# Kernel optimization log

Hardware: AMD Instinct MI355X
Metric: run time of the kernel (lower is better)

## Reference

```python
import jax, jax.numpy as jnp
import numpy as np

B, SEQ, NVAR, DM, K = 2, 512, 64, 128, 2
SCALE = DM ** -0.5  # ScaledDotProductAttention scale, lsa=False so constant


def _period_branch(x4, Wel, bel, Wq, bq, Wk, bk, Wv, bv, Wo, bo, period):
    # x4: [B, DM(time), NVAR, DM(dim)] -- output of start_embed
    pad = (-DM) % period
    pn = (DM + pad) // period  # period_num
    xp = jnp.pad(x4, ((0, 0), (0, pad), (0, 0), (0, 0)))
    # torch .unfold(dim=1, size=period, step=period) -> [B, pn, NVAR, DM, period]
    xw = xp.reshape(B, pn, period, NVAR, DM).transpose(0, 1, 3, 4, 2)
    # emb_linear over the d_model (dim) axis
    xw = jnp.einsum('bqndl,ed->bqnel', xw, Wel) + bel[None, None, None, :, None]
    # -> [B, NVAR, dim, pn, period] then flatten to conv1d layout [bn, dim, L]
    X = xw.transpose(0, 2, 3, 1, 4).reshape(B * NVAR, DM, pn * period)
    # 1x1 Conv1d QKV projections over the channel (dim) axis
    q = jnp.einsum('bdl,ed->bel', X, Wq) + bq[None, :, None]
    k = jnp.einsum('bdl,ed->bel', X, Wk) + bk[None, :, None]
    v = jnp.einsum('bdl,ed->bel', X, Wv) + bv[None, :, None]
    q_s = q.reshape(B * NVAR, DM, pn, period).transpose(0, 1, 3, 2)  # [bn,dim,pl,pn]
    k_s = k.reshape(B * NVAR, DM, pn, period)                         # [bn,dim,pn,pl]
    v_s = v.reshape(B * NVAR, DM, pn, period).transpose(0, 1, 3, 2)  # [bn,dim,pl,pn]
    attn = jax.nn.softmax(jnp.einsum('bdip,bdpj->bdij', q_s, k_s) * SCALE, axis=-1)
    o = jnp.einsum('bdij,bdjp->bdip', attn, v_s)  # [bn, dim, period, pn]
    o = o.reshape(B * NVAR, DM, period * pn)[:, :, :DM]  # truncate to n_heads=DM
    return o @ Wo.T + bo  # to_out Linear(n_heads, n_heads), dropout eval-mode


def reference(x, W_emb, b_emb, W_start, b_start, Wel, bel, Wq, bq, Wk, bk, Wv, bv, Wo, bo, f1, f2):
    # inverted embedding: Linear(seq_len->d_model) over time, then permute -> [B, DM, NVAR]
    xe = (jnp.einsum('bsn,sd->bnd', x, W_emb) + b_emb).transpose(0, 2, 1)
    # FFT_for_Period amplitudes; top-k frequency indices f1,f2 are static (host-side in torch)
    amp = jnp.abs(jnp.fft.rfft(xe, axis=1)).mean(-1)  # [B, DM//2+1]
    pw = jax.nn.softmax(jnp.stack([amp[:, f1], amp[:, f2]], -1), axis=-1)  # [B, K]
    # start_embed: Linear(1 -> d_model) -> [B, DM, NVAR, DM]
    x4 = xe[..., None] * W_start + b_start
    outs = [_period_branch(x4, Wel, bel, Wq, bq, Wk, bk, Wv, bv, Wo, bo, DM // f)
            for f in (f1, f2)]
    res = jnp.stack(outs, -1)                      # [B*NVAR, DM, DM, K]
    pw_b = jnp.repeat(pw, NVAR, axis=0)            # [B*NVAR, K] (b-major order matches reshape)
    out = (res * pw_b[:, None, None, :]).sum(-1)
    return out.reshape(B, NVAR, DM, DM)


def setup_inputs() -> dict:
    key = jax.random.key(0)
    ks = jax.random.split(key, 16)
    s = 0.02
    d = {
        'x': jax.random.normal(ks[0], (B, SEQ, NVAR), jnp.float32),
        'W_emb': jax.random.normal(ks[1], (SEQ, DM), jnp.float32) * s,
        'b_emb': jax.random.normal(ks[2], (DM,), jnp.float32) * s,
        'W_start': jax.random.normal(ks[3], (DM,), jnp.float32) * s,
        'b_start': jax.random.normal(ks[4], (DM,), jnp.float32) * s,
        'Wel': jax.random.normal(ks[5], (DM, DM), jnp.float32) * s,
        'bel': jax.random.normal(ks[6], (DM,), jnp.float32) * s,
        'Wq': jax.random.normal(ks[7], (DM, DM), jnp.float32) * s,
        'bq': jax.random.normal(ks[8], (DM,), jnp.float32) * s,
        'Wk': jax.random.normal(ks[9], (DM, DM), jnp.float32) * s,
        'bk': jax.random.normal(ks[10], (DM,), jnp.float32) * s,
        'Wv': jax.random.normal(ks[11], (DM, DM), jnp.float32) * s,
        'bv': jax.random.normal(ks[12], (DM,), jnp.float32) * s,
        'Wo': jax.random.normal(ks[13], (DM, DM), jnp.float32) * s,
        'bo': jax.random.normal(ks[14], (DM,), jnp.float32) * s,
    }
    # host-side FFT period detection, mirroring torch's .detach().cpu().numpy() topk
    xe = np.einsum('bsn,sd->bnd', np.asarray(d['x']), np.asarray(d['W_emb'])) + np.asarray(d['b_emb'])
    xe = xe.transpose(0, 2, 1)  # [B, DM, NVAR]
    fl = np.abs(np.fft.rfft(xe, axis=1)).mean(0).mean(-1)
    fl[0] = 0.0
    top = np.argsort(-fl, kind='stable')[:K]
    d['f1'] = int(top[0])
    d['f2'] = int(top[1])
    return d
```

## Files before the change

### kernel.cpp

```cpp
#include <hip/hip_runtime.h>

#define DMD 128
#define NV 64
#define BB 2
#define SQ 512
#define NBN 128
#define ASCALE 0.08838834764831845f
#define L2E 1.4426950408889634f
#define CSC (ASCALE * L2E)

#define WS_XE  0
#define WS_PW  (WS_XE + NBN*DMD)
#define WS_VEC (WS_PW + 4)
#define WS_OB  (WS_VEC + 9*DMD)

__global__ __launch_bounds__(512) void k_xe(const float* __restrict__ x,
                                            const float* __restrict__ W_emb,
                                            const float* __restrict__ b_emb,
                                            float* __restrict__ ws) {
    int bn = blockIdx.x;
    int b = bn >> 6, n = bn & 63;
    int tid = threadIdx.x;
    int t = tid & 127, sc = tid >> 7;
    __shared__ float xsh[SQ];
    __shared__ float part[3][DMD];
    xsh[tid] = x[(b * SQ + tid) * NV + n];
    __syncthreads();
    float acc = 0.f;
    const float* W = W_emb + (sc * 128) * DMD + t;
#pragma unroll 8
    for (int s = 0; s < 128; ++s) acc = fmaf(xsh[sc * 128 + s], W[s * DMD], acc);
    if (sc) part[sc - 1][t] = acc;
    __syncthreads();
    if (sc == 0)
        ws[WS_XE + bn * DMD + t] = acc + part[0][t] + part[1][t] + part[2][t] + b_emb[t];
}

__global__ __launch_bounds__(128) void k_prep(const int* __restrict__ f1p,
                                              const int* __restrict__ f2p,
                                              const float* __restrict__ Wel, const float* __restrict__ bel,
                                              const float* __restrict__ W_start, const float* __restrict__ b_start,
                                              const float* __restrict__ Wq, const float* __restrict__ bq,
                                              const float* __restrict__ Wk, const float* __restrict__ bk,
                                              const float* __restrict__ Wv, const float* __restrict__ bv,
                                              float* __restrict__ ws) {
    int tid = threadIdx.x;
    __shared__ float ct[DMD], st[DMD];
    __shared__ float a2[2];
    __shared__ float A[DMD], C[DMD], BL[DMD];
    if (blockIdx.x < 2) {
        int b = blockIdx.x;
        float ang = (float)tid * 0.04908738521234052f;
        ct[tid] = cosf(ang);
        st[tid] = sinf(ang);
        __syncthreads();
        int k = tid >> 6;
        int n = tid & 63;
        int f = k ? f2p[0] : f1p[0];
        const float* xr = ws + WS_XE + (b * NV + n) * DMD;
        float re = 0.f, im = 0.f;
        for (int t = 0; t < DMD; ++t) {
            int ph = (f * t) & (DMD - 1);
            float v = xr[t];
            re = fmaf(v, ct[ph], re);
            im = fmaf(v, st[ph], im);
        }
        float amp = sqrtf(re * re + im * im);
        for (int off = 32; off > 0; off >>= 1) amp += __shfl_down(amp, off);
        if (n == 0) a2[k] = amp * (1.0f / NV);
        __syncthreads();
        if (tid == 0) {
            float m = fmaxf(a2[0], a2[1]);
            float e0 = expf(a2[0] - m), e1 = expf(a2[1] - m);
            float inv = 1.0f / (e0 + e1);
            ws[WS_PW + b * 2 + 0] = e0 * inv;
            ws[WS_PW + b * 2 + 1] = e1 * inv;
        }
    } else {
        int e = tid;
        float a = 0.f, c = 0.f;
        for (int d = 0; d < DMD; ++d) {
            float w = Wel[e * DMD + d];
            a = fmaf(w, W_start[d], a);
            c = fmaf(w, b_start[d], c);
        }
        A[e] = a;
        C[e] = c + bel[e];
        BL[e] = bel[e];
        __syncthreads();
        float aq = 0, cq = 0, pq = 0, ak = 0, ck = 0, pk = 0, av = 0, cv = 0, pv = 0;
        for (int d = 0; d < DMD; ++d) {
            float Ad = A[d], Cd = C[d], Bd = BL[d];
            float wq = Wq[e * DMD + d], wk = Wk[e * DMD + d], wv = Wv[e * DMD + d];
            aq = fmaf(wq, Ad, aq); cq = fmaf(wq, Cd, cq); pq = fmaf(wq, Bd, pq);
            ak = fmaf(wk, Ad, ak); ck = fmaf(wk, Cd, ck); pk = fmaf(wk, Bd, pk);
            av = fmaf(wv, Ad, av); cv = fmaf(wv, Cd, cv); pv = fmaf(wv, Bd, pv);
        }
        float* V = ws + WS_VEC;
        V[0 * DMD + e] = aq; V[1 * DMD + e] = cq + bq[e]; V[2 * DMD + e] = pq + bq[e];
        V[3 * DMD + e] = ak; V[4 * DMD + e] = ck + bk[e]; V[5 * DMD + e] = pk + bk[e];
        V[6 * DMD + e] = av; V[7 * DMD + e] = cv + bv[e]; V[8 * DMD + e] = pv + bv[e];
    }
}


__device__ __forceinline__ void attn_rank1(int br, float pwv, const float (*Vsh)[4],
                                           const float* xs, float (*obuf)[132], int tid) {
    float xi = xs[tid];
    float t[4], l[4], ax[4];
#pragma unroll
    for (int k = 0; k < 4; ++k) {
        float Aq = Vsh[0][k], Cq = Vsh[1][k], Ak = Vsh[3][k];
        t[k] = CSC * fmaf(xi, Aq, Cq) * Ak;
        l[k] = 0.f; ax[k] = 0.f;
    }
#pragma unroll 4
    for (int j = 0; j < DMD; ++j) {
        float xj = xs[j];
#pragma unroll
        for (int k = 0; k < 4; ++k) {
            float ev = exp2f(t[k] * xj);
            l[k] += ev;
            ax[k] = fmaf(ev, xj, ax[k]);
        }
    }
#pragma unroll
    for (int k = 0; k < 4; ++k) {
        float Av = Vsh[6][k], Cv = Vsh[7][k];
        float o = fmaf(Av, ax[k] / l[k], Cv);
        float val = pwv * o;
        if (br == 0) obuf[k][tid] = val; else obuf[k][tid] += val;
    }
}

template<int PP, int NP>
__device__ __forceinline__ void attn_pow2(int br, float pwv, const float (*Vsh)[4],
                                          const float* xs, float (*obuf)[132], int tid) {
    const int UH = PP / 4;
    int lane4 = tid & 3, i0 = tid >> 2, jb = lane4 * UH;

    float xq[NP][UH], U2[UH];
#pragma unroll
    for (int u = 0; u < UH; ++u) {
        int j = jb + u;
        float s = 0.f;
#pragma unroll
        for (int q = 0; q < NP; ++q) { float xv = xs[q * PP + j]; xq[q][u] = xv; s += xv; }
        U2[u] = s;
    }
    const int NREP = (PP == 64) ? 2 : 1;
#pragma unroll
    for (int rep = 0; rep < NREP; ++rep) {
        int i = i0 + rep * 32;
        float G2[UH];
#pragma unroll
        for (int u = 0; u < UH; ++u) G2[u] = 0.f;
#pragma unroll
        for (int q = 0; q < NP; ++q) {
            float xi = xs[q * PP + i];
#pragma unroll
            for (int u = 0; u < UH; ++u) G2[u] = fmaf(xi, xq[q][u], G2[u]);
        }
        for (int ec = 0; ec < 4; ++ec) {
            float Aq = Vsh[0][ec], Cq = Vsh[1][ec];
            float Ak = Vsh[3][ec];
            float Av = Vsh[6][ec], Cv = Vsh[7][ec];
            float t = CSC * Ak;
            float d1 = t * Aq, d2 = t * Cq;
            float l0 = 0.f, l1 = 0.f;
            float accq[NP];
#pragma unroll
            for (int q = 0; q < NP; ++q) accq[q] = 0.f;
#pragma unroll
            for (int u = 0; u < UH; ++u) {
                float ev = exp2f(fmaf(d1, G2[u], d2 * U2[u]));
                if (u & 1) l1 += ev; else l0 += ev;
#pragma unroll
                for (int q = 0; q < NP; ++q) accq[q] = fmaf(ev, xq[q][u], accq[q]);
            }
            float l = l0 + l1;
            l += __shfl_xor(l, 1); l += __shfl_xor(l, 2);
#pragma unroll
            for (int q = 0; q < NP; ++q) {
                accq[q] += __shfl_xor(accq[q], 1);
                accq[q] += __shfl_xor(accq[q], 2);
            }
            if (lane4 == 0) {
                float li = 1.f / l;
#pragma unroll
                for (int q = 0; q < NP; ++q) {
                    float o = fmaf(Av, accq[q] * li, Cv);
                    float val = pwv * o;
                    int mo = i * NP + q;
                    if (br == 0) obuf[ec][mo] = val; else obuf[ec][mo] += val;
                }
            }
        }
    }
}

template<int UB>
__device__ __forceinline__ void attn_small(
    int P, int pn, int r, int Prows, int br, float pwv,
    const float (*Vsh)[4], const float* xs, const float* U, const float* xt,
    float* W, float (*obuf)[132], int tid)
{
    int GP = P + 1;
    int tot = Prows * P;
    unsigned mP = (4096u + (unsigned)P - 1u) / (unsigned)P;
    unsigned mpn = (4096u + (unsigned)pn - 1u) / (unsigned)pn;

    bool v0 = (tid < tot);
    int i0 = (int)(((unsigned)tid * mP) >> 12);
    int j0 = tid - i0 * P;
    bool A0 = (i0 < r), c0 = (j0 < r);
    float xtj0 = xt[j0], Uj0 = U[j0];
    float xti0 = A0 ? xt[i0] : 0.f;
    float g0 = 0.f;
    for (int p = 0; p < pn - 1; ++p) g0 = fmaf(xs[p * P + i0], xs[p * P + j0], g0);
    float Gx0 = (A0 && c0) ? fmaf(xti0, xtj0, g0) : g0;
    float Ux0 = (A0 && c0) ? Uj0 + xtj0 : Uj0;
    float Xw0 = (!A0 && c0) ? xtj0 : 0.f;
    float mw0 = c0 ? 1.f : 0.f;
    int wa0 = i0 * GP + j0;

    int idx1 = tid + 128;
    bool v1 = (idx1 < tot);
    int idx1c = v1 ? idx1 : 0;
    int i1 = (int)(((unsigned)idx1c * mP) >> 12);
    int j1 = idx1c - i1 * P;
    bool A1 = (i1 < r), c1 = (j1 < r);
    float xtj1 = xt[j1], Uj1 = U[j1];
    float xti1 = A1 ? xt[i1] : 0.f;
    float g1 = 0.f;
    for (int p = 0; p < pn - 1; ++p) g1 = fmaf(xs[p * P + i1], xs[p * P + j1], g1);
    float Gx1 = (A1 && c1) ? fmaf(xti1, xtj1, g1) : g1;
    float Ux1 = (A1 && c1) ? Uj1 + xtj1 : Uj1;
    float Xw1 = (!A1 && c1) ? xtj1 : 0.f;
    float mw1 = c1 ? 1.f : 0.f;
    int wa1 = i1 * GP + j1;

    int i2 = (int)(((unsigned)tid * mpn) >> 12);
    int p2 = tid - i2 * pn;
    bool lastp = (p2 == pn - 1);
    int row2 = i2 * GP;
    float xsr[UB];
#pragma unroll
    for (int j = 0; j < UB; ++j) {
        int idx = p2 * P + j;
        xsr[j] = (j < P && idx < DMD) ? xs[idx] : 0.f;
    }

    for (int ec = 0; ec < 4; ++ec) {
        float Aq = Vsh[0][ec], Cq = Vsh[1][ec], Pq = Vsh[2][ec];
        float Ak = Vsh[3][ec], Ck = Vsh[4][ec], Pk = Vsh[5][ec];
        float Av = Vsh[6][ec], Cv = Vsh[7][ec], Pv = Vsh[8][ec];
        float t = CSC * Ak;
        float d1 = t * Aq, d2 = t * Cq, d3 = t * Pq;
        float ckpk = CSC * (Ck - Pk);

        if (v0) {
            float aS = A0 ? fmaf(Aq, xti0, Cq) : Pq;
            float S = (ckpk * aS) * mw0;
            S = fmaf(d3, Xw0, S);
            S = fmaf(d2, Ux0, S);
            S = fmaf(d1, Gx0, S);
            W[wa0] = exp2f(S);
        }
        if (v1) {
            float aS = A1 ? fmaf(Aq, xti1, Cq) : Pq;
            float S = (ckpk * aS) * mw1;
            S = fmaf(d3, Xw1, S);
            S = fmaf(d2, Ux1, S);
            S = fmaf(d1, Gx1, S);
            W[wa1] = exp2f(S);
        }
        __syncthreads();
        float l = 0.f, wr = 0.f, ax = 0.f;
#pragma unroll
        for (int j = 0; j < UB; ++j) {
            float w = W[row2 + ((j < P) ? j : 0)];
            w = (j < P) ? w : 0.f;
            l += w;
            wr += (j < r) ? w : 0.f;
            ax = fmaf(w, xsr[j], ax);
        }
        float li = 1.f / l;
        float o;
        if (lastp) { float sl = wr * li; o = fmaf(Av, ax * li, fmaf(Cv, sl, Pv * (1.f - sl))); }
        else       o = fmaf(Av, ax * li, Cv);
        float val = pwv * o;
        if (br == 0) obuf[ec][tid] = val; else obuf[ec][tid] += val;
        __syncthreads();
    }
}

template<int UH, int NP>
__device__ __forceinline__ void attn_midA(
    int P, int pn, int r, int Prows, int br, float pwv,
    const float (*Vsh)[4], const float* xs, const float* U,
    const float* xt, float (*obuf)[132], int tid)
{
    int lane4 = tid & 3;
    int i0 = tid >> 2;
    int jb = lane4 * UH;

    float Ur[UH], xtr[UH], xq0[UH], xq1[UH];
#pragma unroll
    for (int u = 0; u < UH; ++u) {
        int j = jb + u, jc = (j < P) ? j : 0;
        Ur[u] = U[jc];
        xtr[u] = xt[jc];
        xq0[u] = (j < DMD) ? xs[j] : 0.f;
        int i1x = P + j;
        xq1[u] = (i1x < DMD) ? xs[i1x] : 0.f;
    }
    int nrep = (Prows > 32) ? 2 : 1;
    for (int rep = 0; rep < nrep; ++rep) {
        int i = i0 + rep * 32;
        bool rowact = (i < Prows);
        int ic = rowact ? i : 0;
        float xtic = xt[ic];
        bool rowvalid = (ic < r);
        float g[UH];
#pragma unroll
        for (int u = 0; u < UH; ++u) g[u] = 0.f;
        for (int p = 0; p < pn - 1; ++p) {
            float xi = xs[p * P + ic];
#pragma unroll
            for (int u = 0; u < UH; ++u) {
                int j = jb + u, jc = (j < P) ? j : 0;
                g[u] = fmaf(xi, xs[p * P + jc], g[u]);
            }
        }
        for (int ec = 0; ec < 4; ++ec) {
            float Aq = Vsh[0][ec], Cq = Vsh[1][ec], Pq = Vsh[2][ec];
            float Ak = Vsh[3][ec], Ck = Vsh[4][ec], Pk = Vsh[5][ec];
            float Av = Vsh[6][ec], Cv = Vsh[7][ec], Pv = Vsh[8][ec];
            float c1 = CSC * Aq * Ak, c3 = CSC * Cq * Ak;
            float asi = CSC * (rowvalid ? fmaf(xtic, Aq, Cq) : Pq);

            float l0 = 0.f, l1 = 0.f, w0 = 0.f, w1 = 0.f;
            float accq[NP];
#pragma unroll
            for (int q = 0; q < NP; ++q) accq[q] = 0.f;
#pragma unroll
            for (int u = 0; u < UH; ++u) {
                int j = jb + u;
                float bK = (j < r) ? fmaf(xtr[u], Ak, Ck) : Pk;
                float S = fmaf(asi, bK, fmaf(c3, Ur[u], c1 * g[u]));
                float ev = exp2f(S);
                ev = (j < P) ? ev : 0.f;
                if (u & 1) l1 += ev; else l0 += ev;
                float evr = (j < r) ? ev : 0.f;
                if (u & 1) w1 += evr; else w0 += evr;
                accq[0] = fmaf(ev, xq0[u], accq[0]);
                if (NP >= 2) accq[1] = fmaf(ev, xq1[u], accq[1]);
#pragma unroll
                for (int q = 2; q < NP; ++q) {
                    int idx = q * P + j;
                    float xv = (idx < DMD) ? xs[idx] : 0.f;
                    accq[q] = fmaf(ev, xv, accq[q]);
                }
            }
            float l = l0 + l1, wr = w0 + w1;
            l += __shfl_xor(l, 1);  l += __shfl_xor(l, 2);
            wr += __shfl_xor(wr, 1); wr += __shfl_xor(wr, 2);
#pragma unroll
            for (int q = 0; q < NP; ++q) {
                if (q < pn) {
                    accq[q] += __shfl_xor(accq[q], 1);
                    accq[q] += __shfl_xor(accq[q], 2);
                }
            }
            if (lane4 == 0 && rowact) {
                float li = 1.f / l;
#pragma unroll
                for (int q = 0; q < NP; ++q) {
                    if (q < pn) {
                        int mo = i * pn + q;
                        if (mo < DMD) {
                            float o;
                            if (q == pn - 1) {
                                float sl = wr * li;
                                o = fmaf(Av, accq[q] * li, fmaf(Cv, sl, Pv * (1.f - sl)));
                            } else {
                                o = fmaf(Av, accq[q] * li, Cv);
                            }
                            float val = pwv * o;
                            if (br == 0) obuf[ec][mo] = val;
                            else         obuf[ec][mo] += val;
                        }
                    }
                }
            }
        }
    }
}

__global__ __launch_bounds__(128) void k_attn(const int* __restrict__ f1p,
                                              const int* __restrict__ f2p,
                                              float* __restrict__ ws) {
    int bn = blockIdx.y, b = bn >> 6;
    int e0 = blockIdx.x * 4;
    int tid = threadIdx.x;

    __shared__ float xs[DMD], U[64], xt[64];
    __shared__ float Vsh[9][4];
    __shared__ float W[288];
    __shared__ float obuf[4][132];

    xs[tid] = ws[WS_XE + bn * DMD + tid];
    if (tid < 36) Vsh[tid >> 2][tid & 3] = ws[WS_VEC + (tid >> 2) * DMD + e0 + (tid & 3)];
    int fv0 = f1p[0], fv1 = f2p[0];
    float pw0 = ws[WS_PW + b * 2 + 0];
    float pw1 = ws[WS_PW + b * 2 + 1];
    __syncthreads();

    for (int br = 0; br < 2; ++br) {
        int f = br ? fv1 : fv0;
        float pwv = br ? pw1 : pw0;
        int P = DMD / f;
        int pn = (DMD + P - 1) / P;
        int r = DMD - (pn - 1) * P;
        int Prows = (DMD + pn - 1) / pn;

        if (br == 1) __syncthreads();

        if (P == DMD) {
            attn_rank1(br, pwv, Vsh, xs, obuf, tid);
        } else {
            if (tid < P) {
                float s = 0.f;
                for (int p = 0; p < pn - 1; ++p) s += xs[p * P + tid];
                U[tid] = s;
                xt[tid] = (tid < r) ? xs[(pn - 1) * P + tid] : 0.f;
            }
            __syncthreads();
            if (P <= 4)       attn_small<4>(P, pn, r, Prows, br, pwv, Vsh, xs, U, xt, W, obuf, tid);
            else if (P <= 8)  attn_small<8>(P, pn, r, Prows, br, pwv, Vsh, xs, U, xt, W, obuf, tid);
            else if (P <= 16) attn_small<16>(P, pn, r, Prows, br, pwv, Vsh, xs, U, xt, W, obuf, tid);
            else if (P == 64) attn_pow2<64, 2>(br, pwv, Vsh, xs, obuf, tid);
            else if (P == 32) attn_pow2<32, 4>(br, pwv, Vsh, xs, obuf, tid);
            else if (P > 32)  attn_midA<16, 4>(P, pn, r, Prows, br, pwv, Vsh, xs, U, xt, obuf, tid);
            else              attn_midA<8, 8>(P, pn, r, Prows, br, pwv, Vsh, xs, U, xt, obuf, tid);
        }
    }
    __syncthreads();
    for (int ec = 0; ec < 4; ++ec)
        ws[WS_OB + (bn * DMD + e0 + ec) * DMD + tid] = obuf[ec][tid];
}

__global__ __launch_bounds__(256) void k_out(const float* __restrict__ Wo,
                                             const float* __restrict__ bo,
                                             const float* __restrict__ ws,
                                             float* __restrict__ out) {
    int blk = blockIdx.x;
    int bn0 = (blk >> 2) * 2;
    int e0  = (blk & 3) * 32;
    int tid = threadIdx.x;
    __shared__ __align__(16) float WTc[32 * 132];
    __shared__ __align__(16) float oT[2][32][36];
    int hg = tid & 31, eg = tid >> 5, h0 = hg * 4;

    float acc[2][4][4];
#pragma unroll
    for (int a = 0; a < 2; ++a)
#pragma unroll
        for (int c = 0; c < 4; ++c)
#pragma unroll
            for (int d = 0; d < 4; ++d) acc[a][c][d] = 0.f;

    for (int mc = 0; mc < 4; ++mc) {
        int m0 = mc * 32;
        __syncthreads();
        for (int idx = tid; idx < 4096; idx += 256) {
            int h = idx >> 5, mm = idx & 31;
            WTc[mm * 132 + h] = Wo[h * DMD + m0 + mm];
        }
        for (int idx = tid; idx < 2048; idx += 256) {
            int bnl = idx >> 10, rem = idx & 1023, e = rem >> 5, mm = rem & 31;
            oT[bnl][mm][e] = ws[WS_OB + ((bn0 + bnl) * DMD + e0 + e) * DMD + m0 + mm];
        }
        __syncthreads();
#pragma unroll 4
        for (int mm = 0; mm < 32; ++mm) {
            const float4 wv = *reinterpret_cast<const float4*>(&WTc[mm * 132 + h0]);
            const float4 q0 = *reinterpret_cast<const float4*>(&oT[0][mm][eg * 4]);
            const float4 q1 = *reinterpret_cast<const float4*>(&oT[1][mm][eg * 4]);
            float ae[2][4] = {{q0.x, q0.y, q0.z, q0.w}, {q1.x, q1.y, q1.z, q1.w}};
#pragma unroll
            for (int bnl = 0; bnl < 2; ++bnl) {
#pragma unroll
                for (int el = 0; el < 4; ++el) {
                    float a = ae[bnl][el];
                    acc[bnl][el][0] = fmaf(a, wv.x, acc[bnl][el][0]);
                    acc[bnl][el][1] = fmaf(a, wv.y, acc[bnl][el][1]);
                    acc[bnl][el][2] = fmaf(a, wv.z, acc[bnl][el][2]);
                    acc[bnl][el][3] = fmaf(a, wv.w, acc[bnl][el][3]);
                }
            }
        }
    }
    const float4 bov = *reinterpret_cast<const float4*>(&bo[h0]);
#pragma unroll
    for (int bnl = 0; bnl < 2; ++bnl) {
#pragma unroll
        for (int el = 0; el < 4; ++el) {
            float4 res = { acc[bnl][el][0] + bov.x, acc[bnl][el][1] + bov.y,
                           acc[bnl][el][2] + bov.z, acc[bnl][el][3] + bov.w };
            int e = e0 + eg * 4 + el;
            *reinterpret_cast<float4*>(&out[((bn0 + bnl) * DMD + e) * DMD + h0]) = res;
        }
    }
}

extern "C" void kernel_launch(void* const* d_in, const int* in_sizes, int n_in,
                              void* d_out, int out_size, void* d_ws, size_t ws_size,
                              hipStream_t stream) {
    const float* x       = (const float*)d_in[0];
    const float* W_emb   = (const float*)d_in[1];
    const float* b_emb   = (const float*)d_in[2];
    const float* W_start = (const float*)d_in[3];
    const float* b_start = (const float*)d_in[4];
    const float* Wel     = (const float*)d_in[5];
    const float* bel     = (const float*)d_in[6];
    const float* Wq      = (const float*)d_in[7];
    const float* bq      = (const float*)d_in[8];
    const float* Wk      = (const float*)d_in[9];
    const float* bk      = (const float*)d_in[10];
    const float* Wv      = (const float*)d_in[11];
    const float* bv      = (const float*)d_in[12];
    const float* Wo      = (const float*)d_in[13];
    const float* bo      = (const float*)d_in[14];
    const int*   f1p     = (const int*)d_in[15];
    const int*   f2p     = (const int*)d_in[16];
    float* ws  = (float*)d_ws;
    float* out = (float*)d_out;

    k_xe<<<NBN, 512, 0, stream>>>(x, W_emb, b_emb, ws);
    k_prep<<<3, 128, 0, stream>>>(f1p, f2p, Wel, bel, W_start, b_start,
                                  Wq, bq, Wk, bk, Wv, bv, ws);
    k_attn<<<dim3(32, NBN), 128, 0, stream>>>(f1p, f2p, ws);
    k_out<<<256, 256, 0, stream>>>(Wo, bo, ws, out);
}
```

Baseline: 81.95 us.

## Split attention branches across grid z and write partials directly to global

The two period branches now run in separate blocks along a third grid dimension instead of sequentially in one block. Each branch writes its weighted output straight to global memory, one to the workspace and one to the output buffer, and k_out sums the two partials when loading. attn_small computes all four channels' scores before a single barrier, and attn_pow2 handles several channels per pass. This doubles parallelism and removes shared-memory accumulation and barriers, at the cost of an extra global read in k_out and the output buffer serving as scratch.

```diff
diff --git a/kernel.cpp b/kernel.cpp
--- a/kernel.cpp
+++ b/kernel.cpp
@@ -59,6 +59,7 @@
         int f = k ? f2p[0] : f1p[0];
         const float* xr = ws + WS_XE + (b * NV + n) * DMD;
         float re = 0.f, im = 0.f;
+#pragma unroll 8
         for (int t = 0; t < DMD; ++t) {
             int ph = (f * t) & (DMD - 1);
             float v = xr[t];
@@ -104,8 +105,9 @@
 }
 
 
-__device__ __forceinline__ void attn_rank1(int br, float pwv, const float (*Vsh)[4],
-                                           const float* xs, float (*obuf)[132], int tid) {
+__device__ __forceinline__ void attn_rank1(float pwv, const float (*Vsh)[4],
+                                           const float* xs, float* __restrict__ ob,
+                                           int rowbase, int tid) {
     float xi = xs[tid];
     float t[4], l[4], ax[4];
 #pragma unroll
@@ -128,14 +130,14 @@
     for (int k = 0; k < 4; ++k) {
         float Av = Vsh[6][k], Cv = Vsh[7][k];
         float o = fmaf(Av, ax[k] / l[k], Cv);
-        float val = pwv * o;
-        if (br == 0) obuf[k][tid] = val; else obuf[k][tid] += val;
-    }
-}
-
-template<int PP, int NP>
-__device__ __forceinline__ void attn_pow2(int br, float pwv, const float (*Vsh)[4],
-                                          const float* xs, float (*obuf)[132], int tid) {
+        ob[rowbase + k * DMD + tid] = pwv * o;
+    }
+}
+
+template<int PP, int NP, int EB>
+__device__ __forceinline__ void attn_pow2(float pwv, const float (*Vsh)[4],
+                                          const float* xs, float* __restrict__ ob,
+                                          int rowbase, int tid) {
     const int UH = PP / 4;
     int lane4 = tid & 3, i0 = tid >> 2, jb = lane4 * UH;
 
@@ -161,38 +163,51 @@
 #pragma unroll
             for (int u = 0; u < UH; ++u) G2[u] = fmaf(xi, xq[q][u], G2[u]);
         }
-        for (int ec = 0; ec < 4; ++ec) {
-            float Aq = Vsh[0][ec], Cq = Vsh[1][ec];
-            float Ak = Vsh[3][ec];
-            float Av = Vsh[6][ec], Cv = Vsh[7][ec];
-            float t = CSC * Ak;
-            float d1 = t * Aq, d2 = t * Cq;
-            float l0 = 0.f, l1 = 0.f;
-            float accq[NP];
-#pragma unroll
-            for (int q = 0; q < NP; ++q) accq[q] = 0.f;
+#pragma unroll
+        for (int eg = 0; eg < 4; eg += EB) {
+            float d1[EB], d2[EB], l[EB];
+            float accq[NP][EB];
+#pragma unroll
+            for (int k = 0; k < EB; ++k) {
+                float t = CSC * Vsh[3][eg + k];
+                d1[k] = t * Vsh[0][eg + k];
+                d2[k] = t * Vsh[1][eg + k];
+                l[k] = 0.f;
+#pragma unroll
+                for (int q = 0; q < NP; ++q) accq[q][k] = 0.f;
+            }
 #pragma unroll
             for (int u = 0; u < UH; ++u) {
-                float ev = exp2f(fmaf(d1, G2[u], d2 * U2[u]));
-                if (u & 1) l1 += ev; else l0 += ev;
-#pragma unroll
-                for (int q = 0; q < NP; ++q) accq[q] = fmaf(ev, xq[q][u], accq[q]);
-            }
-            float l = l0 + l1;
-            l += __shfl_xor(l, 1); l += __shfl_xor(l, 2);
-#pragma unroll
-            for (int q = 0; q < NP; ++q) {
-                accq[q] += __shfl_xor(accq[q], 1);
-                accq[q] += __shfl_xor(accq[q], 2);
-            }
+                float gg = G2[u], uu = U2[u];
+                float ev[EB];
+#pragma unroll
+                for (int k = 0; k < EB; ++k) ev[k] = exp2f(fmaf(d1[k], gg, d2[k] * uu));
+#pragma unroll
+                for (int k = 0; k < EB; ++k) {
+                    l[k] += ev[k];
+#pragma unroll
+                    for (int q = 0; q < NP; ++q) accq[q][k] = fmaf(ev[k], xq[q][u], accq[q][k]);
+                }
+            }
+#pragma unroll
+            for (int k = 0; k < EB; ++k) { l[k] += __shfl_xor(l[k], 1); l[k] += __shfl_xor(l[k], 2); }
+#pragma unroll
+            for (int q = 0; q < NP; ++q)
+#pragma unroll
+                for (int k = 0; k < EB; ++k) {
+                    accq[q][k] += __shfl_xor(accq[q][k], 1);
+                    accq[q][k] += __shfl_xor(accq[q][k], 2);
+                }
             if (lane4 == 0) {
-                float li = 1.f / l;
-#pragma unroll
-                for (int q = 0; q < NP; ++q) {
-                    float o = fmaf(Av, accq[q] * li, Cv);
-                    float val = pwv * o;
-                    int mo = i * NP + q;
-                    if (br == 0) obuf[ec][mo] = val; else obuf[ec][mo] += val;
+#pragma unroll
+                for (int k = 0; k < EB; ++k) {
+                    float li = 1.f / l[k];
+                    float Av = Vsh[6][eg + k], Cv = Vsh[7][eg + k];
+#pragma unroll
+                    for (int q = 0; q < NP; ++q) {
+                        float o = fmaf(Av, accq[q][k] * li, Cv);
+                        ob[rowbase + (eg + k) * DMD + i * NP + q] = pwv * o;
+                    }
                 }
             }
         }
@@ -201,9 +216,9 @@
 
 template<int UB>
 __device__ __forceinline__ void attn_small(
-    int P, int pn, int r, int Prows, int br, float pwv,
+    int P, int pn, int r, int Prows, float pwv,
     const float (*Vsh)[4], const float* xs, const float* U, const float* xt,
-    float* W, float (*obuf)[132], int tid)
+    float* W, float* __restrict__ ob, int rowbase, int tid)
 {
     int GP = P + 1;
     int tot = Prows * P;
@@ -251,35 +266,35 @@
         xsr[j] = (j < P && idx < DMD) ? xs[idx] : 0.f;
     }
 
+    float s[4][2];
+#pragma unroll
     for (int ec = 0; ec < 4; ++ec) {
         float Aq = Vsh[0][ec], Cq = Vsh[1][ec], Pq = Vsh[2][ec];
         float Ak = Vsh[3][ec], Ck = Vsh[4][ec], Pk = Vsh[5][ec];
-        float Av = Vsh[6][ec], Cv = Vsh[7][ec], Pv = Vsh[8][ec];
         float t = CSC * Ak;
         float d1 = t * Aq, d2 = t * Cq, d3 = t * Pq;
         float ckpk = CSC * (Ck - Pk);
-
-        if (v0) {
-            float aS = A0 ? fmaf(Aq, xti0, Cq) : Pq;
-            float S = (ckpk * aS) * mw0;
-            S = fmaf(d3, Xw0, S);
-            S = fmaf(d2, Ux0, S);
-            S = fmaf(d1, Gx0, S);
-            W[wa0] = exp2f(S);
-        }
-        if (v1) {
-            float aS = A1 ? fmaf(Aq, xti1, Cq) : Pq;
-            float S = (ckpk * aS) * mw1;
-            S = fmaf(d3, Xw1, S);
-            S = fmaf(d2, Ux1, S);
-            S = fmaf(d1, Gx1, S);
-            W[wa1] = exp2f(S);
-        }
-        __syncthreads();
+        float aS0 = A0 ? fmaf(Aq, xti0, Cq) : Pq;
+        s[ec][0] = fmaf(d1, Gx0, fmaf(d2, Ux0, fmaf(d3, Xw0, (ckpk * aS0) * mw0)));
+        float aS1 = A1 ? fmaf(Aq, xti1, Cq) : Pq;
+        s[ec][1] = fmaf(d1, Gx1, fmaf(d2, Ux1, fmaf(d3, Xw1, (ckpk * aS1) * mw1)));
+    }
+#pragma unroll
+    for (int ec = 0; ec < 4; ++ec) { s[ec][0] = exp2f(s[ec][0]); s[ec][1] = exp2f(s[ec][1]); }
+#pragma unroll
+    for (int ec = 0; ec < 4; ++ec) {
+        if (v0) W[ec * 288 + wa0] = s[ec][0];
+        if (v1) W[ec * 288 + wa1] = s[ec][1];
+    }
+    __syncthreads();
+
+#pragma unroll
+    for (int ec = 0; ec < 4; ++ec) {
+        float Av = Vsh[6][ec], Cv = Vsh[7][ec], Pv = Vsh[8][ec];
         float l = 0.f, wr = 0.f, ax = 0.f;
 #pragma unroll
         for (int j = 0; j < UB; ++j) {
-            float w = W[row2 + ((j < P) ? j : 0)];
+            float w = W[ec * 288 + row2 + ((j < P) ? j : 0)];
             w = (j < P) ? w : 0.f;
             l += w;
             wr += (j < r) ? w : 0.f;
@@ -289,17 +304,15 @@
         float o;
         if (lastp) { float sl = wr * li; o = fmaf(Av, ax * li, fmaf(Cv, sl, Pv * (1.f - sl))); }
         else       o = fmaf(Av, ax * li, Cv);
-        float val = pwv * o;
-        if (br == 0) obuf[ec][tid] = val; else obuf[ec][tid] += val;
-        __syncthreads();
+        ob[rowbase + ec * DMD + tid] = pwv * o;
     }
 }
 
 template<int UH, int NP>
 __device__ __forceinline__ void attn_midA(
-    int P, int pn, int r, int Prows, int br, float pwv,
+    int P, int pn, int r, int Prows, float pwv,
     const float (*Vsh)[4], const float* xs, const float* U,
-    const float* xt, float (*obuf)[132], int tid)
+    const float* xt, float* __restrict__ ob, int rowbase, int tid)
 {
     int lane4 = tid & 3;
     int i0 = tid >> 2;
@@ -387,9 +400,7 @@
                             } else {
                                 o = fmaf(Av, accq[q] * li, Cv);
                             }
-                            float val = pwv * o;
-                            if (br == 0) obuf[ec][mo] = val;
-                            else         obuf[ec][mo] += val;
+                            ob[rowbase + ec * DMD + mo] = pwv * o;
                         }
                     }
                 }
@@ -400,55 +411,49 @@
 
 __global__ __launch_bounds__(128) void k_attn(const int* __restrict__ f1p,
                                               const int* __restrict__ f2p,
-                                              float* __restrict__ ws) {
+                                              float* __restrict__ ws,
+                                              float* __restrict__ outb) {
     int bn = blockIdx.y, b = bn >> 6;
     int e0 = blockIdx.x * 4;
+    int br = blockIdx.z;
     int tid = threadIdx.x;
 
     __shared__ float xs[DMD], U[64], xt[64];
     __shared__ float Vsh[9][4];
-    __shared__ float W[288];
-    __shared__ float obuf[4][132];
+    __shared__ float W[4 * 288];
 
     xs[tid] = ws[WS_XE + bn * DMD + tid];
     if (tid < 36) Vsh[tid >> 2][tid & 3] = ws[WS_VEC + (tid >> 2) * DMD + e0 + (tid & 3)];
-    int fv0 = f1p[0], fv1 = f2p[0];
-    float pw0 = ws[WS_PW + b * 2 + 0];
-    float pw1 = ws[WS_PW + b * 2 + 1];
+    int f = br ? f2p[0] : f1p[0];
+    float pwv = ws[WS_PW + b * 2 + br];
+    float* ob = br ? outb : (ws + WS_OB);
+    int rowbase = (bn * DMD + e0) * DMD;
     __syncthreads();
 
-    for (int br = 0; br < 2; ++br) {
-        int f = br ? fv1 : fv0;
-        float pwv = br ? pw1 : pw0;
-        int P = DMD / f;
-        int pn = (DMD + P - 1) / P;
-        int r = DMD - (pn - 1) * P;
-        int Prows = (DMD + pn - 1) / pn;
-
-        if (br == 1) __syncthreads();
-
-        if (P == DMD) {
-            attn_rank1(br, pwv, Vsh, xs, obuf, tid);
-        } else {
-            if (tid < P) {
-                float s = 0.f;
-                for (int p = 0; p < pn - 1; ++p) s += xs[p * P + tid];
-                U[tid] = s;
-                xt[tid] = (tid < r) ? xs[(pn - 1) * P + tid] : 0.f;
-            }
-            __syncthreads();
-            if (P <= 4)       attn_small<4>(P, pn, r, Prows, br, pwv, Vsh, xs, U, xt, W, obuf, tid);
-            else if (P <= 8)  attn_small<8>(P, pn, r, Prows, br, pwv, Vsh, xs, U, xt, W, obuf, tid);
-            else if (P <= 16) attn_small<16>(P, pn, r, Prows, br, pwv, Vsh, xs, U, xt, W, obuf, tid);
-            else if (P == 64) attn_pow2<64, 2>(br, pwv, Vsh, xs, obuf, tid);
-            else if (P == 32) attn_pow2<32, 4>(br, pwv, Vsh, xs, obuf, tid);
-            else if (P > 32)  attn_midA<16, 4>(P, pn, r, Prows, br, pwv, Vsh, xs, U, xt, obuf, tid);
-            else              attn_midA<8, 8>(P, pn, r, Prows, br, pwv, Vsh, xs, U, xt, obuf, tid);
-        }
+    int P = DMD / f;
+    int pn = (DMD + P - 1) / P;
+    int r = DMD - (pn - 1) * P;
+    int Prows = (DMD + pn - 1) / pn;
+
+    if (P == DMD) {
+        attn_rank1(pwv, Vsh, xs, ob, rowbase, tid);
+        return;
+    }
+    if (tid < P) {
+        float s = 0.f;
+        for (int p = 0; p < pn - 1; ++p) s += xs[p * P + tid];
+        U[tid] = s;
+        xt[tid] = (tid < r) ? xs[(pn - 1) * P + tid] : 0.f;
     }
     __syncthreads();
-    for (int ec = 0; ec < 4; ++ec)
-        ws[WS_OB + (bn * DMD + e0 + ec) * DMD + tid] = obuf[ec][tid];
+
+    if (P <= 4)       attn_small<4>(P, pn, r, Prows, pwv, Vsh, xs, U, xt, W, ob, rowbase, tid);
+    else if (P <= 8)  attn_small<8>(P, pn, r, Prows, pwv, Vsh, xs, U, xt, W, ob, rowbase, tid);
+    else if (P <= 16) attn_small<16>(P, pn, r, Prows, pwv, Vsh, xs, U, xt, W, ob, rowbase, tid);
+    else if (P == 64) attn_pow2<64, 2, 2>(pwv, Vsh, xs, ob, rowbase, tid);
+    else if (P == 32) attn_pow2<32, 4, 4>(pwv, Vsh, xs, ob, rowbase, tid);
+    else if (P > 32)  attn_midA<16, 4>(P, pn, r, Prows, pwv, Vsh, xs, U, xt, ob, rowbase, tid);
+    else              attn_midA<8, 8>(P, pn, r, Prows, pwv, Vsh, xs, U, xt, ob, rowbase, tid);
 }
 
 __global__ __launch_bounds__(256) void k_out(const float* __restrict__ Wo,
@@ -480,7 +485,8 @@
         }
         for (int idx = tid; idx < 2048; idx += 256) {
             int bnl = idx >> 10, rem = idx & 1023, e = rem >> 5, mm = rem & 31;
-            oT[bnl][mm][e] = ws[WS_OB + ((bn0 + bnl) * DMD + e0 + e) * DMD + m0 + mm];
+            int gi = ((bn0 + bnl) * DMD + e0 + e) * DMD + m0 + mm;
+            oT[bnl][mm][e] = ws[WS_OB + gi] + out[gi];
         }
         __syncthreads();
 #pragma unroll 4
@@ -541,6 +547,6 @@
     k_xe<<<NBN, 512, 0, stream>>>(x, W_emb, b_emb, ws);
     k_prep<<<3, 128, 0, stream>>>(f1p, f2p, Wel, bel, W_start, b_start,
                                   Wq, bq, Wk, bk, Wv, bv, ws);
-    k_attn<<<dim3(32, NBN), 128, 0, stream>>>(f1p, f2p, ws);
+    k_attn<<<dim3(32, NBN, 2), 128, 0, stream>>>(f1p, f2p, ws, out);
     k_out<<<256, 256, 0, stream>>>(Wo, bo, ws, out);
 }
```

Result: slower. 86.28 us (+5.3%).
